# Optimization experiments

Measured on AMD Instinct MI355X. Metric: run time of the kernel, lower is better.

The kernel has to match this reference:

```python
import jax, jax.numpy as jnp
import numpy as np

B, N, DEG, RATIO = 100, 1000, 16, 0.8
E = B * N * DEG                      # 1.6M edges
K1 = int(np.ceil(RATIO * N))         # 800
K2 = int(np.ceil(RATIO * K1))        # 640
K3 = int(np.ceil(RATIO * K2))        # 512
F_IN, H, OUT = 128, 128, 10


def _graph_conv(x, src, dst, emask, w_root, w_rel, b):
    # PyG GraphConv (aggr='add'): out = lin_rel(sum_j x_j) + lin_root(x) + bias
    msg = x[src] * emask[:, None].astype(x.dtype)               # [E, F]
    agg = jax.ops.segment_sum(msg, dst, num_segments=x.shape[0])
    return agg @ w_rel.T + x @ w_root.T + b


def _topk_pool(x, src, dst, emask, w, n_per_graph, k):
    # PyG TopKPooling: score = tanh((x.w)/||w||); keep top-k per graph; x *= score
    score = jnp.tanh((x @ w) / jnp.linalg.norm(w))              # [B*n]
    vals, idx = jax.lax.top_k(score.reshape(B, n_per_graph), k)  # [B,k]
    perm = (idx + jnp.arange(B)[:, None] * n_per_graph).reshape(-1)
    new_x = x[perm] * vals.reshape(-1, 1)
    mapping = jnp.full(B * n_per_graph, -1, dtype=jnp.int32).at[perm].set(
        jnp.arange(B * k, dtype=jnp.int32))
    ns, nd = mapping[src], mapping[dst]
    valid = emask & (ns >= 0) & (nd >= 0)
    return new_x, jnp.where(valid, ns, 0), jnp.where(valid, nd, 0), valid


def _global_pool(x, k):
    xg = x.reshape(B, k, x.shape[-1])
    return jnp.concatenate([xg.max(axis=1), xg.mean(axis=1)], axis=1)  # [B, 2H]


def setup_inputs() -> dict:
    key = jax.random.key(0)
    ks = jax.random.split(key, 16)
    x = jax.random.normal(ks[0], (B * N, F_IN), jnp.float32)
    src = jax.random.randint(ks[1], (B, N * DEG), 0, N)
    dst = jax.random.randint(ks[2], (B, N * DEG), 0, N)
    off = (jnp.arange(B) * N)[:, None]
    edge_index = jnp.stack([(src + off).reshape(-1), (dst + off).reshape(-1)])

    def lin(k, fo, fi):
        return jax.random.normal(k, (fo, fi), jnp.float32) / np.sqrt(fi).astype(np.float32)

    return {
        'x': x, 'edge_index': edge_index,
        'w_root1': lin(ks[3], H, F_IN), 'w_rel1': lin(ks[4], H, F_IN), 'b1': jnp.zeros((H,), jnp.float32),
        'pw1': jax.random.normal(ks[5], (H,), jnp.float32),
        'w_root2': lin(ks[6], H, H), 'w_rel2': lin(ks[7], H, H), 'b2': jnp.zeros((H,), jnp.float32),
        'pw2': jax.random.normal(ks[8], (H,), jnp.float32),
        'w_root3': lin(ks[9], H, H), 'w_rel3': lin(ks[10], H, H), 'b3': jnp.zeros((H,), jnp.float32),
        'pw3': jax.random.normal(ks[11], (H,), jnp.float32),
        'lin1_w': lin(ks[12], 128, 256), 'lin1_b': jnp.zeros((128,), jnp.float32),
        'lin2_w': lin(ks[13], 64, 128), 'lin2_b': jnp.zeros((64,), jnp.float32),
        'lin3_w': lin(ks[14], OUT, 64), 'lin3_b': jnp.zeros((OUT,), jnp.float32),
    }


def reference(x, edge_index, w_root1, w_rel1, b1, pw1, w_root2, w_rel2, b2, pw2,
              w_root3, w_rel3, b3, pw3, lin1_w, lin1_b, lin2_w, lin2_b, lin3_w, lin3_b):
    src, dst = edge_index[0], edge_index[1]
    emask = jnp.ones(src.shape[0], dtype=bool)

    h = jax.nn.relu(_graph_conv(x, src, dst, emask, w_root1, w_rel1, b1))
    h, src, dst, emask = _topk_pool(h, src, dst, emask, pw1, N, K1)
    x1 = _global_pool(h, K1)

    h = jax.nn.relu(_graph_conv(h, src, dst, emask, w_root2, w_rel2, b2))
    h, src, dst, emask = _topk_pool(h, src, dst, emask, pw2, K1, K2)
    x2 = _global_pool(h, K2)

    h = jax.nn.relu(_graph_conv(h, src, dst, emask, w_root3, w_rel3, b3))
    h, src, dst, emask = _topk_pool(h, src, dst, emask, pw3, K2, K3)
    x3 = _global_pool(h, K3)

    g = x1 + x2 + x3                                   # [B, 256]
    g = jax.nn.relu(g @ lin1_w.T + lin1_b)             # dropout: eval mode (identity)
    g = jax.nn.relu(g @ lin2_w.T + lin2_b)
    return jax.nn.log_softmax(g @ lin3_w.T + lin3_b, axis=-1)
```

## Files before the change

### kernel.cpp

```cpp
#include <hip/hip_runtime.h>
#include <math.h>

constexpr int BG = 100;
constexpr int NN = 1000;
constexpr int EE = 1600000;
constexpr int NV = 100000;
constexpr int FD = 128;
constexpr int K1 = 800, K2 = 640, K3 = 512;

__device__ __forceinline__ float xla_tanh(float x) {
    const float kClamp = 7.90531110763549805f;
    const float a1 = 4.89352455891786e-03f, a3 = 6.37261928875436e-04f,
                a5 = 1.48572235717979e-05f, a7 = 5.12229709037114e-08f,
                a9 = -8.60467152213735e-11f, a11 = 2.00018790482477e-13f,
                a13 = -2.76076847742355e-16f;
    const float b0 = 4.89352518554385e-03f, b2 = 2.26843463243900e-03f,
                b4 = 1.18534705686654e-04f, b6 = 1.19825839466702e-06f;
    if (fabsf(x) < 4e-04f) return x;
    float xc = fminf(fmaxf(x, -kClamp), kClamp);
    float x2 = xc * xc;
    float p = fmaf(x2, a13, a11);
    p = fmaf(x2, p, a9);
    p = fmaf(x2, p, a7);
    p = fmaf(x2, p, a5);
    p = fmaf(x2, p, a3);
    p = fmaf(x2, p, a1);
    p = xc * p;
    float q = fmaf(x2, b6, b4);
    q = fmaf(x2, q, b2);
    q = fmaf(x2, q, b0);
    return p / q;
}

__global__ __launch_bounds__(256) void zero_k(int* __restrict__ p, int n) {
    int i = blockIdx.x * 256 + threadIdx.x;
    if (i < n) p[i] = 0;
}
__global__ __launch_bounds__(256) void count_k(const int* __restrict__ dst,
                                               int* __restrict__ cnt) {
    int e = blockIdx.x * 256 + threadIdx.x;
    if (e < EE) atomicAdd(&cnt[dst[e]], 1);
}
__global__ __launch_bounds__(1024) void scan1_k(const int* __restrict__ cnt,
                                                int* __restrict__ excl,
                                                int* __restrict__ bsum, int n) {
    __shared__ int s[1024];
    int b = blockIdx.x, t = threadIdx.x, i = b * 1024 + t;
    int v = (i < n) ? cnt[i] : 0;
    s[t] = v; __syncthreads();
    for (int off = 1; off < 1024; off <<= 1) {
        int x = (t >= off) ? s[t - off] : 0;
        __syncthreads();
        s[t] += x;
        __syncthreads();
    }
    if (i < n) excl[i] = s[t] - v;
    if (t == 1023) bsum[b] = s[t];
}
__global__ void scan2_k(int* __restrict__ bsum, int nb) {
    if (threadIdx.x == 0) {
        int acc = 0;
        for (int b = 0; b < nb; ++b) { int v = bsum[b]; bsum[b] = acc; acc += v; }
    }
}
__global__ __launch_bounds__(256) void scan3_k(int* __restrict__ rowptr,
                                               const int* __restrict__ bsum,
                                               int* __restrict__ cursor, int n) {
    int i = blockIdx.x * 256 + threadIdx.x;
    if (i < n) {
        int v = rowptr[i] + bsum[i >> 10];
        rowptr[i] = v;
        cursor[i] = v;
    }
    if (i == 0) rowptr[n] = EE;
}
__global__ __launch_bounds__(256) void fill_k(const int* __restrict__ dst,
                                              int* __restrict__ cursor,
                                              int* __restrict__ eidx) {
    int e = blockIdx.x * 256 + threadIdx.x;
    if (e < EE) {
        int p = atomicAdd(&cursor[dst[e]], 1);
        eidx[p] = e;
    }
}
__global__ __launch_bounds__(256) void compose_k(const int* __restrict__ m1,
                                                 const int* __restrict__ m2,
                                                 int* __restrict__ cm, int n) {
    int i = blockIdx.x * 256 + threadIdx.x;
    if (i < n) { int v = m1[i]; cm[i] = (v < 0) ? -1 : m2[v]; }
}

__global__ __launch_bounds__(128) void gather2_k(
    const float* __restrict__ feat, const int* __restrict__ src,
    const int* __restrict__ rowptr, const int* __restrict__ eidx,
    const int* __restrict__ map, float* __restrict__ agg)
{
    __shared__ int sS[96];
    int d = blockIdx.x, f = threadIdx.x;
    int dm = d;
    if (map) { dm = map[d]; if (dm < 0) return; }
    int beg = rowptr[d], end = rowptr[d + 1];
    double acc = 0.0;
    while (beg < end) {
        int chunk = min(96, end - beg);
        if (f < chunk) {
            int s = src[eidx[beg + f]];
            if (map) s = map[s];
            sS[f] = s;
        }
        __syncthreads();
        for (int i = 0; i < chunk; ++i) {
            int s = sS[i];
            if (s >= 0) acc += (double)feat[(size_t)s * FD + f];
        }
        __syncthreads();
        beg += chunk;
    }
    agg[(size_t)dm * FD + f] = (float)acc;
}

constexpr int TR = 32;
constexpr int LDK = 132;
__global__ __launch_bounds__(128) void conv_mm2(
    const float* __restrict__ in, float* __restrict__ agg,
    const float* __restrict__ w_root, const float* __restrict__ w_rel,
    const float* __restrict__ bias)
{
    __shared__ float sA[TR][LDK];
    __shared__ float sI[TR][LDK];
    int r0 = blockIdx.x * TR;
    int t = threadIdx.x;
    #pragma unroll
    for (int q = 0; q < 8; ++q) {
        int idx = q * 128 + t;
        int row = idx >> 5, c4 = idx & 31;
        float4 va = *(const float4*)(agg + (size_t)(r0 + row) * FD + c4 * 4);
        float4 vi = *(const float4*)(in  + (size_t)(r0 + row) * FD + c4 * 4);
        *(float4*)&sA[row][c4 * 4] = va;
        *(float4*)&sI[row][c4 * 4] = vi;
    }
    __syncthreads();
    int g  = t >> 6;
    int cp = t & 63;
    const float* wr0 = w_rel  + (size_t)(2 * cp) * FD;
    const float* wr1 = wr0 + FD;
    const float* wo0 = w_root + (size_t)(2 * cp) * FD;
    const float* wo1 = wo0 + FD;
    float acc[2][16];
    #pragma unroll
    for (int c = 0; c < 2; ++c)
        #pragma unroll
        for (int r = 0; r < 16; ++r) acc[c][r] = 0.f;
    for (int k0 = 0; k0 < FD; k0 += 4) {
        float4 r0v = *(const float4*)(wr0 + k0);
        float4 r1v = *(const float4*)(wr1 + k0);
        float4 o0v = *(const float4*)(wo0 + k0);
        float4 o1v = *(const float4*)(wo1 + k0);
        #pragma unroll
        for (int r = 0; r < 16; ++r) {
            float4 a = *(const float4*)&sA[g * 16 + r][k0];
            float4 b = *(const float4*)&sI[g * 16 + r][k0];
            acc[0][r] += a.x * r0v.x + b.x * o0v.x;
            acc[0][r] += a.y * r0v.y + b.y * o0v.y;
            acc[0][r] += a.z * r0v.z + b.z * o0v.z;
            acc[0][r] += a.w * r0v.w + b.w * o0v.w;
            acc[1][r] += a.x * r1v.x + b.x * o1v.x;
            acc[1][r] += a.y * r1v.y + b.y * o1v.y;
            acc[1][r] += a.z * r1v.z + b.z * o1v.z;
            acc[1][r] += a.w * r1v.w + b.w * o1v.w;
        }
    }
    float b0 = bias[2 * cp], b1 = bias[2 * cp + 1];
    __syncthreads();
    #pragma unroll
    for (int r = 0; r < 16; ++r) {
        float v0 = b0 + acc[0][r];
        float v1 = b1 + acc[1][r];
        v0 = v0 > 0.f ? v0 : 0.f;
        v1 = v1 > 0.f ? v1 : 0.f;
        *(float2*)(agg + (size_t)(r0 + g * 16 + r) * FD + 2 * cp) =
            make_float2(v0, v1);
    }
}

__global__ __launch_bounds__(128) void norm_k(const float* __restrict__ pw,
                                              float* __restrict__ nrm)
{
    int t = threadIdx.x;
    float v = pw[t]; v *= v;
    #pragma unroll
    for (int off = 32; off; off >>= 1) v += __shfl_down(v, off);
    __shared__ float s[2];
    if ((t & 63) == 0) s[t >> 6] = v;
    __syncthreads();
    if (t == 0) nrm[0] = sqrtf(s[0] + s[1]);
}

__global__ __launch_bounds__(256) void scores_k(
    const float* __restrict__ h, const float* __restrict__ pw,
    const float* __restrict__ nrm, float* __restrict__ out, int rows)
{
    int gid = blockIdx.x * 256 + threadIdx.x;
    int node = gid >> 6, lane = gid & 63;
    if (node >= rows) return;
    float2 hv = *(const float2*)(h + (size_t)node * FD + lane * 2);
    float2 wv = *(const float2*)(pw + lane * 2);
    double d = (double)hv.x * (double)wv.x + (double)hv.y * (double)wv.y;
    #pragma unroll
    for (int off = 32; off; off >>= 1) d += __shfl_down(d, off);
    if (lane == 0) {
        float arg = (float)d / nrm[0];
        out[node] = xla_tanh(arg);
    }
}

__global__ __launch_bounds__(512) void topk_k(
    const float* __restrict__ h, const float* __restrict__ scores,
    float* __restrict__ outx, int* __restrict__ mapping, int n_per, int k)
{
    __shared__ unsigned long long sk[1024];
    __shared__ int sel[1024];
    int b = blockIdx.x, tid = threadIdx.x;
    for (int i = tid; i < 1024; i += 512) {
        float f = (i < n_per) ? scores[b * n_per + i] : -INFINITY;
        unsigned u = __float_as_uint(f);
        u = (u & 0x80000000u) ? ~u : (u | 0x80000000u);
        sk[i] = ((unsigned long long)u << 32) | (unsigned)(1023 - i);
        sel[i] = -1;
    }
    __syncthreads();
    for (int ksz = 2; ksz <= 1024; ksz <<= 1) {
        for (int j = ksz >> 1; j; j >>= 1) {
            int i = ((tid & ~(j - 1)) << 1) | (tid & (j - 1));
            int p = i | j;
            bool up = ((i & ksz) == 0);
            unsigned long long ki = sk[i], kp = sk[p];
            if ((ki < kp) == up) { sk[i] = kp; sk[p] = ki; }
            __syncthreads();
        }
    }
    for (int i = tid; i < k; i += 512)
        sel[1023 - (unsigned)(sk[i] & 0xFFFFFFFFu)] = i;
    __syncthreads();
    for (int i = tid; i < n_per; i += 512)
        mapping[b * n_per + i] = (sel[i] >= 0) ? b * k + sel[i] : -1;
    for (int t = tid; t < k * 32; t += 512) {
        int nj = t >> 5, f4 = t & 31;
        unsigned long long kk = sk[nj];
        int old = 1023 - (unsigned)(kk & 0xFFFFFFFFu);
        unsigned u = (unsigned)(kk >> 32);
        float val = (u & 0x80000000u) ? __uint_as_float(u & 0x7FFFFFFFu)
                                      : __uint_as_float(~u);
        float4 v = *(const float4*)(h + (size_t)(b * n_per + old) * FD + f4 * 4);
        v.x *= val; v.y *= val; v.z *= val; v.w *= val;
        *(float4*)(outx + (size_t)(b * k + nj) * FD + f4 * 4) = v;
    }
}

__global__ __launch_bounds__(1024) void gpool2_k(const float* __restrict__ xp,
                                                 float* __restrict__ g, int k)
{
    __shared__ float smx[8][128];
    __shared__ float ssm[8][128];
    int b = blockIdx.x, t = threadIdx.x;
    int rg = t >> 7;
    int f  = t & 127;
    float mx = -INFINITY, sm = 0.f;
    for (int j = rg; j < k; j += 8) {
        float v = xp[(size_t)(b * k + j) * FD + f];
        mx = fmaxf(mx, v);
        sm += v;
    }
    smx[rg][f] = mx;
    ssm[rg][f] = sm;
    __syncthreads();
    if (rg == 0) {
        float m = smx[0][f], s = ssm[0][f];
        #pragma unroll
        for (int q = 1; q < 8; ++q) { m = fmaxf(m, smx[q][f]); s += ssm[q][f]; }
        g[b * 256 + f]       += m;
        g[b * 256 + 128 + f] += s * (1.0f / k);
    }
}

__global__ __launch_bounds__(256) void mlp_k(
    const float* __restrict__ g,
    const float* __restrict__ l1w, const float* __restrict__ l1b,
    const float* __restrict__ l2w, const float* __restrict__ l2b,
    const float* __restrict__ l3w, const float* __restrict__ l3b,
    float* __restrict__ out)
{
    __shared__ float s0[256], s1[128], s2[64], s3[10];
    int b = blockIdx.x, t = threadIdx.x;
    s0[t] = g[b * 256 + t];
    __syncthreads();
    if (t < 128) {
        float a = l1b[t];
        for (int kk = 0; kk < 256; ++kk) a += s0[kk] * l1w[t * 256 + kk];
        s1[t] = a > 0.f ? a : 0.f;
    }
    __syncthreads();
    if (t < 64) {
        float a = l2b[t];
        for (int kk = 0; kk < 128; ++kk) a += s1[kk] * l2w[t * 128 + kk];
        s2[t] = a > 0.f ? a : 0.f;
    }
    __syncthreads();
    if (t < 10) {
        float a = l3b[t];
        for (int kk = 0; kk < 64; ++kk) a += s2[kk] * l3w[t * 64 + kk];
        s3[t] = a;
    }
    __syncthreads();
    if (t == 0) {
        float m = s3[0];
        for (int i = 1; i < 10; ++i) m = fmaxf(m, s3[i]);
        float se = 0.f;
        for (int i = 0; i < 10; ++i) se += expf(s3[i] - m);
        float lse = m + logf(se);
        for (int i = 0; i < 10; ++i) out[b * 10 + i] = s3[i] - lse;
    }
}

extern "C" void kernel_launch(void* const* d_in, const int* in_sizes, int n_in,
                              void* d_out, int out_size, void* d_ws, size_t ws_size,
                              hipStream_t stream)
{
    const float* x       = (const float*)d_in[0];
    const int*   ei      = (const int*)d_in[1];
    const int*   src     = ei;
    const int*   dst     = ei + EE;
    const float* w_root1 = (const float*)d_in[2];
    const float* w_rel1  = (const float*)d_in[3];
    const float* b1      = (const float*)d_in[4];
    const float* pw1     = (const float*)d_in[5];
    const float* w_root2 = (const float*)d_in[6];
    const float* w_rel2  = (const float*)d_in[7];
    const float* b2      = (const float*)d_in[8];
    const float* pw2     = (const float*)d_in[9];
    const float* w_root3 = (const float*)d_in[10];
    const float* w_rel3  = (const float*)d_in[11];
    const float* b3      = (const float*)d_in[12];
    const float* pw3     = (const float*)d_in[13];
    const float* l1w     = (const float*)d_in[14];
    const float* l1b     = (const float*)d_in[15];
    const float* l2w     = (const float*)d_in[16];
    const float* l2b     = (const float*)d_in[17];
    const float* l3w     = (const float*)d_in[18];
    const float* l3b     = (const float*)d_in[19];
    float* out = (float*)d_out;

    float* A      = (float*)d_ws;
    float* Bf     = A + (size_t)NV * FD;
    float* scores = Bf + (size_t)80000 * FD;
    float* g      = scores + NV;
    float* nrm    = g + BG * 256;
    int*   map1   = (int*)(nrm + 64);
    int*   map2   = map1 + NV;
    int*   map3   = map2 + 80000;
    int*   rowptr = map3 + 64000;
    int*   cursor = rowptr + NV + 2;
    int*   bsum   = cursor + NV;
    int*   eidx   = bsum + 128;
    int*   cmap   = eidx + EE;

    const int NB_E = (EE + 255) / 256;
    const int NB_V = (NV + 255) / 256;
    const int NB_S = (NV + 1023) / 1024;

    zero_k<<<NB_V, 256, 0, stream>>>(cursor, NV);
    count_k<<<NB_E, 256, 0, stream>>>(dst, cursor);
    scan1_k<<<NB_S, 1024, 0, stream>>>(cursor, rowptr, bsum, NV);
    scan2_k<<<1, 64, 0, stream>>>(bsum, NB_S);
    scan3_k<<<NB_V, 256, 0, stream>>>(rowptr, bsum, cursor, NV);
    fill_k<<<NB_E, 256, 0, stream>>>(dst, cursor, eidx);

    hipMemsetAsync(g, 0, (size_t)BG * 256 * sizeof(float), stream);

    gather2_k<<<NV, 128, 0, stream>>>(x, src, rowptr, eidx, nullptr, A);
    conv_mm2<<<NV / TR, 128, 0, stream>>>(x, A, w_root1, w_rel1, b1);
    norm_k<<<1, 128, 0, stream>>>(pw1, nrm);
    scores_k<<<NV / 4, 256, 0, stream>>>(A, pw1, nrm, scores, NV);
    topk_k<<<BG, 512, 0, stream>>>(A, scores, Bf, map1, NN, K1);
    gpool2_k<<<BG, 1024, 0, stream>>>(Bf, g, K1);

    gather2_k<<<NV, 128, 0, stream>>>(Bf, src, rowptr, eidx, map1, A);
    conv_mm2<<<(BG * K1) / TR, 128, 0, stream>>>(Bf, A, w_root2, w_rel2, b2);
    norm_k<<<1, 128, 0, stream>>>(pw2, nrm);
    scores_k<<<(BG * K1) / 4, 256, 0, stream>>>(A, pw2, nrm, scores, BG * K1);
    topk_k<<<BG, 512, 0, stream>>>(A, scores, Bf, map2, K1, K2);
    gpool2_k<<<BG, 1024, 0, stream>>>(Bf, g, K2);

    compose_k<<<NB_V, 256, 0, stream>>>(map1, map2, cmap, NV);
    gather2_k<<<NV, 128, 0, stream>>>(Bf, src, rowptr, eidx, cmap, A);
    conv_mm2<<<(BG * K2) / TR, 128, 0, stream>>>(Bf, A, w_root3, w_rel3, b3);
    norm_k<<<1, 128, 0, stream>>>(pw3, nrm);
    scores_k<<<(BG * K2) / 4, 256, 0, stream>>>(A, pw3, nrm, scores, BG * K2);
    topk_k<<<BG, 512, 0, stream>>>(A, scores, Bf, map3, K2, K3);
    gpool2_k<<<BG, 1024, 0, stream>>>(Bf, g, K3);

    mlp_k<<<BG, 256, 0, stream>>>(g, l1w, l1b, l2w, l2b, l3w, l3b, out);
}
```

Baseline: 1.123 ms.

## Vectorize neighbor gather with float4 slots and shrink conv matmul tile

The gather kernel now splits 128 threads into 4 edge slots of 32 lanes, each lane loading a float4 of the source row. It keeps four double accumulators and reduces the slots through shared memory. This replaces one scalar load per thread per edge with wider loads and four-way edge parallelism, aiming to cut per-edge latency on the gather-bound aggregation. Separately, the conv matmul row tile drops from 32 to 16 rows to launch more blocks and use fewer registers, at the cost of reloading weights more often. The summation order changes, but the double accumulation should keep results stable.

After: 1.134 ms. About the same (+1.0%).

```diff
diff --git a/kernel.cpp b/kernel.cpp
--- a/kernel.cpp
+++ b/kernel.cpp
@@ -90,38 +90,55 @@
     if (i < n) { int v = m1[i]; cm[i] = (v < 0) ? -1 : m2[v]; }
 }
 
-__global__ __launch_bounds__(128) void gather2_k(
+__global__ __launch_bounds__(128) void gather3_k(
     const float* __restrict__ feat, const int* __restrict__ src,
     const int* __restrict__ rowptr, const int* __restrict__ eidx,
     const int* __restrict__ map, float* __restrict__ agg)
 {
-    __shared__ int sS[96];
-    int d = blockIdx.x, f = threadIdx.x;
+    __shared__ int sS[128];
+    __shared__ double sred[4][32][4];
+    int d = blockIdx.x, t = threadIdx.x;
+    int slot = t >> 5;
+    int fg   = t & 31;
     int dm = d;
     if (map) { dm = map[d]; if (dm < 0) return; }
     int beg = rowptr[d], end = rowptr[d + 1];
-    double acc = 0.0;
+    double a0 = 0.0, a1 = 0.0, a2 = 0.0, a3 = 0.0;
     while (beg < end) {
-        int chunk = min(96, end - beg);
-        if (f < chunk) {
-            int s = src[eidx[beg + f]];
+        int chunk = min(128, end - beg);
+        if (t < chunk) {
+            int s = src[eidx[beg + t]];
             if (map) s = map[s];
-            sS[f] = s;
+            sS[t] = s;
         }
         __syncthreads();
-        for (int i = 0; i < chunk; ++i) {
+        for (int i = slot; i < chunk; i += 4) {
             int s = sS[i];
-            if (s >= 0) acc += (double)feat[(size_t)s * FD + f];
+            if (s >= 0) {
+                float4 v = *(const float4*)(feat + (size_t)s * FD + fg * 4);
+                a0 += (double)v.x; a1 += (double)v.y;
+                a2 += (double)v.z; a3 += (double)v.w;
+            }
         }
         __syncthreads();
         beg += chunk;
     }
-    agg[(size_t)dm * FD + f] = (float)acc;
-}
-
-constexpr int TR = 32;
+    sred[slot][fg][0] = a0; sred[slot][fg][1] = a1;
+    sred[slot][fg][2] = a2; sred[slot][fg][3] = a3;
+    __syncthreads();
+    if (slot == 0) {
+        double r0 = sred[0][fg][0] + sred[1][fg][0] + sred[2][fg][0] + sred[3][fg][0];
+        double r1 = sred[0][fg][1] + sred[1][fg][1] + sred[2][fg][1] + sred[3][fg][1];
+        double r2 = sred[0][fg][2] + sred[1][fg][2] + sred[2][fg][2] + sred[3][fg][2];
+        double r3 = sred[0][fg][3] + sred[1][fg][3] + sred[2][fg][3] + sred[3][fg][3];
+        *(float4*)(agg + (size_t)dm * FD + fg * 4) =
+            make_float4((float)r0, (float)r1, (float)r2, (float)r3);
+    }
+}
+
+constexpr int TR = 16;
 constexpr int LDK = 132;
-__global__ __launch_bounds__(128) void conv_mm2(
+__global__ __launch_bounds__(128) void conv_mm3(
     const float* __restrict__ in, float* __restrict__ agg,
     const float* __restrict__ w_root, const float* __restrict__ w_rel,
     const float* __restrict__ bias)
@@ -131,7 +148,7 @@
     int r0 = blockIdx.x * TR;
     int t = threadIdx.x;
     #pragma unroll
-    for (int q = 0; q < 8; ++q) {
+    for (int q = 0; q < 4; ++q) {
         int idx = q * 128 + t;
         int row = idx >> 5, c4 = idx & 31;
         float4 va = *(const float4*)(agg + (size_t)(r0 + row) * FD + c4 * 4);
@@ -146,20 +163,20 @@
     const float* wr1 = wr0 + FD;
     const float* wo0 = w_root + (size_t)(2 * cp) * FD;
     const float* wo1 = wo0 + FD;
-    float acc[2][16];
+    float acc[2][8];
     #pragma unroll
     for (int c = 0; c < 2; ++c)
         #pragma unroll
-        for (int r = 0; r < 16; ++r) acc[c][r] = 0.f;
+        for (int r = 0; r < 8; ++r) acc[c][r] = 0.f;
     for (int k0 = 0; k0 < FD; k0 += 4) {
         float4 r0v = *(const float4*)(wr0 + k0);
         float4 r1v = *(const float4*)(wr1 + k0);
         float4 o0v = *(const float4*)(wo0 + k0);
         float4 o1v = *(const float4*)(wo1 + k0);
         #pragma unroll
-        for (int r = 0; r < 16; ++r) {
-            float4 a = *(const float4*)&sA[g * 16 + r][k0];
-            float4 b = *(const float4*)&sI[g * 16 + r][k0];
+        for (int r = 0; r < 8; ++r) {
+            float4 a = *(const float4*)&sA[g * 8 + r][k0];
+            float4 b = *(const float4*)&sI[g * 8 + r][k0];
             acc[0][r] += a.x * r0v.x + b.x * o0v.x;
             acc[0][r] += a.y * r0v.y + b.y * o0v.y;
             acc[0][r] += a.z * r0v.z + b.z * o0v.z;
@@ -173,12 +190,12 @@
     float b0 = bias[2 * cp], b1 = bias[2 * cp + 1];
     __syncthreads();
     #pragma unroll
-    for (int r = 0; r < 16; ++r) {
+    for (int r = 0; r < 8; ++r) {
         float v0 = b0 + acc[0][r];
         float v1 = b1 + acc[1][r];
         v0 = v0 > 0.f ? v0 : 0.f;
         v1 = v1 > 0.f ? v1 : 0.f;
-        *(float2*)(agg + (size_t)(r0 + g * 16 + r) * FD + 2 * cp) =
+        *(float2*)(agg + (size_t)(r0 + g * 8 + r) * FD + 2 * cp) =
             make_float2(v0, v1);
     }
 }
@@ -377,23 +394,23 @@
 
     hipMemsetAsync(g, 0, (size_t)BG * 256 * sizeof(float), stream);
 
-    gather2_k<<<NV, 128, 0, stream>>>(x, src, rowptr, eidx, nullptr, A);
-    conv_mm2<<<NV / TR, 128, 0, stream>>>(x, A, w_root1, w_rel1, b1);
+    gather3_k<<<NV, 128, 0, stream>>>(x, src, rowptr, eidx, nullptr, A);
+    conv_mm3<<<NV / TR, 128, 0, stream>>>(x, A, w_root1, w_rel1, b1);
     norm_k<<<1, 128, 0, stream>>>(pw1, nrm);
     scores_k<<<NV / 4, 256, 0, stream>>>(A, pw1, nrm, scores, NV);
     topk_k<<<BG, 512, 0, stream>>>(A, scores, Bf, map1, NN, K1);
     gpool2_k<<<BG, 1024, 0, stream>>>(Bf, g, K1);
 
-    gather2_k<<<NV, 128, 0, stream>>>(Bf, src, rowptr, eidx, map1, A);
-    conv_mm2<<<(BG * K1) / TR, 128, 0, stream>>>(Bf, A, w_root2, w_rel2, b2);
+    gather3_k<<<NV, 128, 0, stream>>>(Bf, src, rowptr, eidx, map1, A);
+    conv_mm3<<<(BG * K1) / TR, 128, 0, stream>>>(Bf, A, w_root2, w_rel2, b2);
     norm_k<<<1, 128, 0, stream>>>(pw2, nrm);
     scores_k<<<(BG * K1) / 4, 256, 0, stream>>>(A, pw2, nrm, scores, BG * K1);
     topk_k<<<BG, 512, 0, stream>>>(A, scores, Bf, map2, K1, K2);
     gpool2_k<<<BG, 1024, 0, stream>>>(Bf, g, K2);
 
     compose_k<<<NB_V, 256, 0, stream>>>(map1, map2, cmap, NV);
-    gather2_k<<<NV, 128, 0, stream>>>(Bf, src, rowptr, eidx, cmap, A);
-    conv_mm2<<<(BG * K2) / TR, 128, 0, stream>>>(Bf, A, w_root3, w_rel3, b3);
+    gather3_k<<<NV, 128, 0, stream>>>(Bf, src, rowptr, eidx, cmap, A);
+    conv_mm3<<<(BG * K2) / TR, 128, 0, stream>>>(Bf, A, w_root3, w_rel3, b3);
     norm_k<<<1, 128, 0, stream>>>(pw3, nrm);
     scores_k<<<(BG * K2) / 4, 256, 0, stream>>>(A, pw3, nrm, scores, BG * K2);
     topk_k<<<BG, 512, 0, stream>>>(A, scores, Bf, map3, K2, K3);
```
